# Kernel tuning notes

Hardware: AMD Instinct MI355X
Metric: run time of the kernel (lower is better)

## Reference

```python
import jax, jax.numpy as jnp
import numpy as np

EXP_CLAMP = 1.0e6
DENOM_EPS = 1e-10
LRELU_ALPHA = 0.01


def setup_inputs() -> dict:
    key = jax.random.key(0)
    k1, k2, k3, k4, k5, k6 = jax.random.split(key, 6)
    B, N, E, F = 4, 16384, 262144, 64
    h = jax.random.normal(k1, (B, N, F), dtype=jnp.float32)
    edge = jax.random.randint(k2, (B, E, 2), 0, N, dtype=jnp.int32)
    edge_num = jax.random.randint(k3, (B,), 1, E, dtype=jnp.int32)
    edge_weight = jax.random.uniform(k4, (B, E), dtype=jnp.float32)
    W = jax.random.normal(k5, (F, F), dtype=jnp.float32) * 0.15  # xavier-ish scale
    a = jax.random.normal(k6, (1, 2 * F), dtype=jnp.float32) * 0.12
    return {"h": h, "edge": edge, "edge_num": edge_num,
            "edge_weight": edge_weight, "W": W, "a": a}


def _seg_sum(src, idx, num_segments):
    # src: [E, ...], idx: [E] -> [num_segments, ...]
    return jax.ops.segment_sum(src, idx, num_segments=num_segments)


def reference(h, edge, edge_num, edge_weight, W, a):
    B, N, Fin = h.shape
    E = edge.shape[1]
    # linear transform: Wh = h @ W^T  -> [B, N, Fout]
    Wh = jnp.einsum('bnf,of->bno', h, W)
    ctr = edge[:, :, 0]  # [B, E]
    nbr = edge[:, :, 1]  # [B, E]
    Wh_c = jnp.take_along_axis(Wh, ctr[:, :, None], axis=1)  # [B, E, Fout]
    Wh_n = jnp.take_along_axis(Wh, nbr[:, :, None], axis=1)  # [B, E, Fout]
    a_input = jnp.concatenate([Wh_c, Wh_n], axis=-1) * edge_weight[:, :, None]
    # attention logits: leakyrelu(a_input @ a^T), squeeze to [B, E]
    att1 = jax.nn.leaky_relu(jnp.einsum('bek,k->be', a_input, a[0]), LRELU_ALPHA)
    # per-batch valid-edge mask (edges beyond edge_num zeroed, as in torch loop)
    mask = (jnp.arange(E, dtype=jnp.int32)[None, :] < edge_num[:, None])
    x_exp = jnp.clip(jnp.exp(att1), 0.0, EXP_CLAMP) * mask.astype(att1.dtype)
    # segment softmax denominator over center nodes
    denom = DENOM_EPS + jax.vmap(_seg_sum, in_axes=(0, 0, None))(x_exp, ctr, N)  # [B, N]
    att = x_exp / jnp.take_along_axis(denom, ctr, axis=1)  # [B, E]
    # weighted neighbor aggregation via scatter-add on center index
    att_Wh = Wh_n * att[:, :, None]  # masked edges already have att == 0
    h_prime = jax.vmap(_seg_sum, in_axes=(0, 0, None))(att_Wh, ctr, N)  # [B, N, Fout]
    return jax.nn.relu(h_prime)
```

## Files before the change

kernel.cpp:

```cpp
#include <hip/hip_runtime.h>

#define BB 4
#define NN 16384
#define EE 262144
#define FF 64
#define ROWS (BB * NN)
#define CAP 64

__device__ __forceinline__ unsigned short f32_to_bf16(float f) {
    unsigned int u = __float_as_uint(f);
    u += 0x7FFFu + ((u >> 16) & 1u);
    return (unsigned short)(u >> 16);
}

__global__ __launch_bounds__(256) void scsn_kernel(
    const float* __restrict__ h, const float* __restrict__ W,
    const float* __restrict__ a,
    float* __restrict__ sc, float* __restrict__ sn, int* __restrict__ cnt)
{
    __shared__ float wc[FF], wn[FF];
    const int t = threadIdx.x;

    if (blockIdx.x < 256) cnt[blockIdx.x * 256 + t] = 0;

    if (t < 128) {
        const int f = t & 63;
        const float* av = a + (t >> 6) * FF;
        float s = 0.0f;
        #pragma unroll 8
        for (int o = 0; o < FF; ++o)
            s = fmaf(av[o], W[o * FF + f], s);
        (t < 64 ? wc : wn)[f] = s;
    }
    __syncthreads();

    const int gl   = t & 15;
    const int rloc = t >> 4;
    const float4 wcv = *(const float4*)&wc[gl * 4];
    const float4 wnv = *(const float4*)&wn[gl * 4];

    for (int base = blockIdx.x * 16; base < ROWS; base += gridDim.x * 16) {
        const int row = base + rloc;
        const float4 hv = ((const float4*)h)[(size_t)row * 16 + gl];
        float s1 = hv.x * wcv.x + hv.y * wcv.y + hv.z * wcv.z + hv.w * wcv.w;
        float s2 = hv.x * wnv.x + hv.y * wnv.y + hv.z * wnv.z + hv.w * wnv.w;
        #pragma unroll
        for (int off = 8; off; off >>= 1) {
            s1 += __shfl_xor(s1, off);
            s2 += __shfl_xor(s2, off);
        }
        if (gl == 0) { sc[row] = s1; sn[row] = s2; }
    }
}

__global__ __launch_bounds__(256) void wh_bin_kernel(
    const float* __restrict__ h, const float* __restrict__ W,
    const int* __restrict__ edge, const int* __restrict__ edge_num,
    const float* __restrict__ ew,
    const float* __restrict__ sc, const float* __restrict__ sn,
    unsigned short* __restrict__ Wh, int* __restrict__ cnt,
    unsigned int* __restrict__ payload)
{
    __shared__ float Wt[FF][68];
    __shared__ float hl[16][65];

    const int t = threadIdx.x;
    for (int i = t; i < FF * FF; i += 256)
        Wt[i & 63][i >> 6] = W[i];

    const int r  = t >> 4;
    const int c4 = (t & 15) * 4;
    for (int tile = blockIdx.x; tile < ROWS / 16; tile += gridDim.x) {
        const int rowBase = tile * 16;
        __syncthreads();
        {
            const float4* hp = (const float4*)(h + (size_t)rowBase * FF);
            float4 v = hp[t];
            hl[t >> 4][(t & 15) * 4]     = v.x;
            hl[t >> 4][(t & 15) * 4 + 1] = v.y;
            hl[t >> 4][(t & 15) * 4 + 2] = v.z;
            hl[t >> 4][(t & 15) * 4 + 3] = v.w;
        }
        __syncthreads();

        float4 acc = {0.f, 0.f, 0.f, 0.f};
        #pragma unroll
        for (int f = 0; f < FF; ++f) {
            const float hv = hl[r][f];
            const float4 w = *(const float4*)&Wt[f][c4];
            acc.x = fmaf(hv, w.x, acc.x);
            acc.y = fmaf(hv, w.y, acc.y);
            acc.z = fmaf(hv, w.z, acc.z);
            acc.w = fmaf(hv, w.w, acc.w);
        }
        ushort4 st = { f32_to_bf16(acc.x), f32_to_bf16(acc.y),
                       f32_to_bf16(acc.z), f32_to_bf16(acc.w) };
        *(ushort4*)(Wh + (size_t)(rowBase + r) * FF + c4) = st;
    }

    for (int i2 = blockIdx.x * 256 + t; i2 < (BB * EE) / 2;
         i2 += gridDim.x * 256) {
        const int b  = i2 >> 17;
        const int e0 = (2 * i2) & (EE - 1);
        const int en = edge_num[b];
        if (e0 >= en) continue;
        const int4   e4 = ((const int4*)edge)[i2];
        const float2 w2 = ((const float2*)ew)[i2];
        const float* snB = sn + b * NN;

        #pragma unroll
        for (int k = 0; k < 2; ++k) {
            if (e0 + k >= en) break;
            const int ctr = k ? e4.z : e4.x;
            const int nbr = k ? e4.w : e4.y;
            const float wgt = k ? w2.y : w2.x;
            const int row = b * NN + ctr;
            float att1 = wgt * (sc[row] + snB[nbr]);
            att1 = att1 > 0.0f ? att1 : 0.01f * att1;
            float xe = fminf(__expf(att1), 1000000.0f);
            unsigned int u = __float_as_uint(xe);
            u = (u + 0x2000u) & 0xFFFFC000u;
            int pos = atomicAdd(&cnt[row], 1);
            if (pos < CAP)
                payload[(size_t)row * CAP + pos] = u | (unsigned int)nbr;
        }
    }
}

__global__ __launch_bounds__(256) void gather_kernel(
    const int* __restrict__ cnt, const unsigned int* __restrict__ payload,
    const uint2* __restrict__ Wh2,
    float* __restrict__ out)
{
    const int bi = blockIdx.x;
    const int xcd = bi & 7;
    const int batch = xcd >> 1;
    const int within = ((bi >> 3) << 1) | (xcd & 1);
    const int rg = batch * 4096 + within;

    const int lane = threadIdx.x & 63;
    const int wave = threadIdx.x >> 6;
    const int row = rg * 4 + wave;
    const int grp = lane >> 4;
    const int gl  = lane & 15;
    int deg = cnt[row];
    if (deg > CAP) deg = CAP;
    const unsigned int* pl = payload + (size_t)row * CAP;
    const uint2* WhB = Wh2 + (size_t)batch * NN * 16;

    float a0 = 0.f, a1 = 0.f, a2 = 0.f, a3 = 0.f, dsum = 0.f;
    const unsigned int p = (lane < deg) ? pl[lane] : 0u;
    for (int jj = 0; jj < deg; jj += 16) {
        const unsigned int pv0 = __shfl(p, jj + grp);
        const unsigned int pv1 = __shfl(p, jj + grp + 4);
        const unsigned int pv2 = __shfl(p, jj + grp + 8);
        const unsigned int pv3 = __shfl(p, jj + grp + 12);
        const uint2 w0 = WhB[(size_t)(pv0 & 0x3FFFu) * 16 + gl];
        const uint2 w1 = WhB[(size_t)(pv1 & 0x3FFFu) * 16 + gl];
        const uint2 w2 = WhB[(size_t)(pv2 & 0x3FFFu) * 16 + gl];
        const uint2 w3 = WhB[(size_t)(pv3 & 0x3FFFu) * 16 + gl];
        const float xe0 = __uint_as_float(pv0 & 0xFFFFC000u);
        const float xe1 = __uint_as_float(pv1 & 0xFFFFC000u);
        const float xe2 = __uint_as_float(pv2 & 0xFFFFC000u);
        const float xe3 = __uint_as_float(pv3 & 0xFFFFC000u);
        a0 = fmaf(xe0, __uint_as_float(w0.x << 16),         a0);
        a1 = fmaf(xe0, __uint_as_float(w0.x & 0xFFFF0000u), a1);
        a2 = fmaf(xe0, __uint_as_float(w0.y << 16),         a2);
        a3 = fmaf(xe0, __uint_as_float(w0.y & 0xFFFF0000u), a3);
        a0 = fmaf(xe1, __uint_as_float(w1.x << 16),         a0);
        a1 = fmaf(xe1, __uint_as_float(w1.x & 0xFFFF0000u), a1);
        a2 = fmaf(xe1, __uint_as_float(w1.y << 16),         a2);
        a3 = fmaf(xe1, __uint_as_float(w1.y & 0xFFFF0000u), a3);
        a0 = fmaf(xe2, __uint_as_float(w2.x << 16),         a0);
        a1 = fmaf(xe2, __uint_as_float(w2.x & 0xFFFF0000u), a1);
        a2 = fmaf(xe2, __uint_as_float(w2.y << 16),         a2);
        a3 = fmaf(xe2, __uint_as_float(w2.y & 0xFFFF0000u), a3);
        a0 = fmaf(xe3, __uint_as_float(w3.x << 16),         a0);
        a1 = fmaf(xe3, __uint_as_float(w3.x & 0xFFFF0000u), a1);
        a2 = fmaf(xe3, __uint_as_float(w3.y << 16),         a2);
        a3 = fmaf(xe3, __uint_as_float(w3.y & 0xFFFF0000u), a3);
        dsum += (xe0 + xe1) + (xe2 + xe3);
    }
    a0 += __shfl_xor(a0, 16); a1 += __shfl_xor(a1, 16);
    a2 += __shfl_xor(a2, 16); a3 += __shfl_xor(a3, 16);
    dsum += __shfl_xor(dsum, 16);
    a0 += __shfl_xor(a0, 32); a1 += __shfl_xor(a1, 32);
    a2 += __shfl_xor(a2, 32); a3 += __shfl_xor(a3, 32);
    dsum += __shfl_xor(dsum, 32);

    if (grp == 0) {
        const float inv = 1.0f / (1e-10f + dsum);
        float4 o;
        o.x = fmaxf(a0 * inv, 0.0f);
        o.y = fmaxf(a1 * inv, 0.0f);
        o.z = fmaxf(a2 * inv, 0.0f);
        o.w = fmaxf(a3 * inv, 0.0f);
        ((float4*)out)[(size_t)row * 16 + gl] = o;
    }
}

extern "C" void kernel_launch(void* const* d_in, const int* in_sizes, int n_in,
                              void* d_out, int out_size, void* d_ws, size_t ws_size,
                              hipStream_t stream)
{
    const float* h        = (const float*)d_in[0];
    const int*   edge     = (const int*)  d_in[1];
    const int*   edge_num = (const int*)  d_in[2];
    const float* ew       = (const float*)d_in[3];
    const float* W        = (const float*)d_in[4];
    const float* a        = (const float*)d_in[5];
    float* out = (float*)d_out;

    unsigned short* Wh = (unsigned short*)d_ws;
    float* sc        = (float*)(Wh + (size_t)BB * NN * FF);
    float* sn        = sc + ROWS;
    int*   cnt       = (int*)(sn + ROWS);
    unsigned int* payload = (unsigned int*)(cnt + ROWS);

    scsn_kernel<<<1024, 256, 0, stream>>>(h, W, a, sc, sn, cnt);

    wh_bin_kernel<<<1024, 256, 0, stream>>>(h, W, edge, edge_num, ew, sc, sn,
                                            Wh, cnt, payload);

    gather_kernel<<<ROWS / 4, 256, 0, stream>>>(cnt, payload,
                                                (const uint2*)Wh, out);
}
```

Before: 140.7 us.

## Register-tile Wh GEMM over 64 rows and issue edge atomics up front

```diff
diff --git a/kernel.cpp b/kernel.cpp
--- a/kernel.cpp
+++ b/kernel.cpp
@@ -62,40 +62,56 @@
     unsigned int* __restrict__ payload)
 {
     __shared__ float Wt[FF][68];
-    __shared__ float hl[16][65];
+    __shared__ float hA[64][65];
 
     const int t = threadIdx.x;
     for (int i = t; i < FF * FF; i += 256)
         Wt[i & 63][i >> 6] = W[i];
 
-    const int r  = t >> 4;
-    const int c4 = (t & 15) * 4;
-    for (int tile = blockIdx.x; tile < ROWS / 16; tile += gridDim.x) {
-        const int rowBase = tile * 16;
+    const int ty = t >> 4;
+    const int tx = t & 15;
+
+    for (int tile = blockIdx.x; tile < ROWS / 64; tile += gridDim.x) {
+        const int rowBase = tile * 64;
         __syncthreads();
         {
             const float4* hp = (const float4*)(h + (size_t)rowBase * FF);
-            float4 v = hp[t];
-            hl[t >> 4][(t & 15) * 4]     = v.x;
-            hl[t >> 4][(t & 15) * 4 + 1] = v.y;
-            hl[t >> 4][(t & 15) * 4 + 2] = v.z;
-            hl[t >> 4][(t & 15) * 4 + 3] = v.w;
+            #pragma unroll
+            for (int k = 0; k < 4; ++k) {
+                const int i4 = t + k * 256;
+                const float4 v = hp[i4];
+                const int rr = i4 >> 4, cc = (i4 & 15) * 4;
+                hA[rr][cc] = v.x; hA[rr][cc + 1] = v.y;
+                hA[rr][cc + 2] = v.z; hA[rr][cc + 3] = v.w;
+            }
         }
         __syncthreads();
 
-        float4 acc = {0.f, 0.f, 0.f, 0.f};
+        float4 acc0 = {0,0,0,0}, acc1 = {0,0,0,0}, acc2 = {0,0,0,0}, acc3 = {0,0,0,0};
         #pragma unroll
         for (int f = 0; f < FF; ++f) {
-            const float hv = hl[r][f];
-            const float4 w = *(const float4*)&Wt[f][c4];
-            acc.x = fmaf(hv, w.x, acc.x);
-            acc.y = fmaf(hv, w.y, acc.y);
-            acc.z = fmaf(hv, w.z, acc.z);
-            acc.w = fmaf(hv, w.w, acc.w);
-        }
-        ushort4 st = { f32_to_bf16(acc.x), f32_to_bf16(acc.y),
-                       f32_to_bf16(acc.z), f32_to_bf16(acc.w) };
-        *(ushort4*)(Wh + (size_t)(rowBase + r) * FF + c4) = st;
+            const float4 wv = *(const float4*)&Wt[f][tx * 4];
+            const float h0 = hA[ty * 4][f];
+            const float h1 = hA[ty * 4 + 1][f];
+            const float h2 = hA[ty * 4 + 2][f];
+            const float h3 = hA[ty * 4 + 3][f];
+            acc0.x = fmaf(h0, wv.x, acc0.x); acc0.y = fmaf(h0, wv.y, acc0.y);
+            acc0.z = fmaf(h0, wv.z, acc0.z); acc0.w = fmaf(h0, wv.w, acc0.w);
+            acc1.x = fmaf(h1, wv.x, acc1.x); acc1.y = fmaf(h1, wv.y, acc1.y);
+            acc1.z = fmaf(h1, wv.z, acc1.z); acc1.w = fmaf(h1, wv.w, acc1.w);
+            acc2.x = fmaf(h2, wv.x, acc2.x); acc2.y = fmaf(h2, wv.y, acc2.y);
+            acc2.z = fmaf(h2, wv.z, acc2.z); acc2.w = fmaf(h2, wv.w, acc2.w);
+            acc3.x = fmaf(h3, wv.x, acc3.x); acc3.y = fmaf(h3, wv.y, acc3.y);
+            acc3.z = fmaf(h3, wv.z, acc3.z); acc3.w = fmaf(h3, wv.w, acc3.w);
+        }
+        const float4 accs[4] = {acc0, acc1, acc2, acc3};
+        #pragma unroll
+        for (int i = 0; i < 4; ++i) {
+            const int row = rowBase + ty * 4 + i;
+            ushort4 st = { f32_to_bf16(accs[i].x), f32_to_bf16(accs[i].y),
+                           f32_to_bf16(accs[i].z), f32_to_bf16(accs[i].w) };
+            *(ushort4*)(Wh + (size_t)row * FF + tx * 4) = st;
+        }
     }
 
     for (int i2 = blockIdx.x * 256 + t; i2 < (BB * EE) / 2;
@@ -106,23 +122,30 @@
         if (e0 >= en) continue;
         const int4   e4 = ((const int4*)edge)[i2];
         const float2 w2 = ((const float2*)ew)[i2];
+        const int row0 = b * NN + e4.x;
+        const int row1 = b * NN + e4.z;
+        const bool act1 = (e0 + 1 < en);
+
+        const int pos0 = atomicAdd(&cnt[row0], 1);
+        const int pos1 = act1 ? atomicAdd(&cnt[row1], 1) : CAP;
+
         const float* snB = sn + b * NN;
-
-        #pragma unroll
-        for (int k = 0; k < 2; ++k) {
-            if (e0 + k >= en) break;
-            const int ctr = k ? e4.z : e4.x;
-            const int nbr = k ? e4.w : e4.y;
-            const float wgt = k ? w2.y : w2.x;
-            const int row = b * NN + ctr;
-            float att1 = wgt * (sc[row] + snB[nbr]);
+        const float sc0 = sc[row0], sn0 = snB[e4.y];
+        float att0 = w2.x * (sc0 + sn0);
+        att0 = att0 > 0.0f ? att0 : 0.01f * att0;
+        const float xe0 = fminf(__expf(att0), 1000000.0f);
+        unsigned int u0 = (__float_as_uint(xe0) + 0x2000u) & 0xFFFFC000u;
+        if (pos0 < CAP)
+            payload[(size_t)row0 * CAP + pos0] = u0 | (unsigned int)e4.y;
+
+        if (act1) {
+            const float sc1 = sc[row1], sn1 = snB[e4.w];
+            float att1 = w2.y * (sc1 + sn1);
             att1 = att1 > 0.0f ? att1 : 0.01f * att1;
-            float xe = fminf(__expf(att1), 1000000.0f);
-            unsigned int u = __float_as_uint(xe);
-            u = (u + 0x2000u) & 0xFFFFC000u;
-            int pos = atomicAdd(&cnt[row], 1);
-            if (pos < CAP)
-                payload[(size_t)row * CAP + pos] = u | (unsigned int)nbr;
+            const float xe1 = fminf(__expf(att1), 1000000.0f);
+            unsigned int u1 = (__float_as_uint(xe1) + 0x2000u) & 0xFFFFC000u;
+            if (pos1 < CAP)
+                payload[(size_t)row1 * CAP + pos1] = u1 | (unsigned int)e4.w;
         }
     }
 }
```

Result: no change. 139.1 us (-1.1%).
